# Optimization experiments

Measured on AMD Instinct MI355X. Metric: run time of the kernel, lower is better.

Reference implementation:

```python
import jax, jax.numpy as jnp
import numpy as np

B, N, E, D, H, L = 1024, 64, 1024, 128, 4, 2
C = D // H          # per-head out_channels
K = 5               # options per attribute
LN_EPS = 1e-5


def setup_inputs() -> dict:
    key = jax.random.key(0)
    ks = jax.random.split(key, 22)
    s = 0.05
    inp = {
        'x': jax.random.randint(ks[0], (B, N), 0, K),
        'edge_index': jax.random.randint(ks[1], (2, E), 0, N),
        'edge_attr': jax.random.uniform(ks[2], (E, 1), jnp.float32),
        # tokenizer params
        'attr_emb': jax.random.normal(ks[3], (N, D), jnp.float32) * s,
        'opt_emb': jax.random.normal(ks[4], (N, K, D), jnp.float32) * s,
        'prior': jnp.ones((N, 1), jnp.float32),
        # GATv2 params, stacked over layers
        'Wl': jax.random.normal(ks[5], (L, D, D), jnp.float32) * s,
        'bl': jnp.zeros((L, D), jnp.float32),
        'Wr': jax.random.normal(ks[6], (L, D, D), jnp.float32) * s,
        'br': jnp.zeros((L, D), jnp.float32),
        'We': jax.random.normal(ks[7], (L, 1, D), jnp.float32) * s,
        'att': jax.random.normal(ks[8], (L, H, C), jnp.float32) * s,
        'conv_bias': jnp.zeros((L, D), jnp.float32),
        'ln_g': jnp.ones((L, D), jnp.float32),
        'ln_b': jnp.zeros((L, D), jnp.float32),
        # reliability head
        'W1': jax.random.normal(ks[9], (2 * D, D), jnp.float32) * s,
        'b1': jnp.zeros((D,), jnp.float32),
        'W2': jax.random.normal(ks[10], (D, 1), jnp.float32) * s,
        'b2': jnp.zeros((1,), jnp.float32),
    }
    return inp


def _forward(x, edge_index, edge_attr, attr_emb, opt_emb, prior,
             Wl, bl, Wr, br, We, att, conv_bias, ln_g, ln_b, W1, b1, W2, b2):
    Bb, n = x.shape
    # Tokenizer: token_i = p_i * (E_attr[i] + E_val[i](x_i))
    val = opt_emb[jnp.arange(n)[None, :], x]                 # [B,n,D]
    T0 = (attr_emb[None] + val) * prior[None]                # [B,n,D]

    src, dst = edge_index[0], edge_index[1]
    h = T0
    for l in range(Wl.shape[0]):
        xl = (h @ Wl[l] + bl[l]).reshape(Bb, n, H, C)        # source transform
        xr = (h @ Wr[l] + br[l]).reshape(Bb, n, H, C)        # target transform
        e = (edge_attr @ We[l]).reshape(1, E, H, C)          # edge embedding
        msg = xl[:, src]                                     # [B,E,H,C]
        z = jax.nn.leaky_relu(msg + xr[:, dst] + e, 0.2)
        alpha = jnp.einsum('behc,hc->beh', z, att[l])        # [B,E,H]
        # segment softmax over incoming edges per target node
        mx = jnp.full((Bb, n, H), -jnp.inf, alpha.dtype).at[:, dst].max(alpha)
        ex = jnp.exp(alpha - mx[:, dst])
        den = jnp.zeros((Bb, n, H), alpha.dtype).at[:, dst].add(ex)
        a = ex / den[:, dst]                                 # normalized attention
        out = jnp.zeros((Bb, n, H, C), h.dtype).at[:, dst].add(msg * a[..., None])
        g = out.reshape(Bb, n, D) + conv_bias[l]
        mu = g.mean(-1, keepdims=True)
        var = g.var(-1, keepdims=True)
        g = (g - mu) / jnp.sqrt(var + LN_EPS) * ln_g[l] + ln_b[l]
        g = jax.nn.elu(g)
        h = h + g                                            # residual

    hat_T = jnp.concatenate([T0, h], axis=-1)                # [B,n,2D]
    rel = jax.nn.sigmoid(jax.nn.relu(hat_T @ W1 + b1) @ W2 + b2)[..., 0]  # [B,n]
    rw = rel[..., None]
    f_scale = (h * rw).sum(1) / (rw.sum(1) + 1e-8)           # [B,D]
    return f_scale, rel, hat_T


def reference(x, edge_index, edge_attr, attr_emb, opt_emb, prior,
              Wl, bl, Wr, br, We, att, conv_bias, ln_g, ln_b, W1, b1, W2, b2):
    return _forward(x, edge_index, edge_attr, attr_emb, opt_emb, prior,
                    Wl, bl, Wr, br, We, att, conv_bias, ln_g, ln_b, W1, b1, W2, b2)
```

## Files before the change

kernel.cpp:

```cpp
#include <hip/hip_runtime.h>
#include <hip/hip_bf16.h>

#define Bv 1024
#define Nv 64
#define Ev 1024
#define Dv 128
#define Hv 4
#define Lv 2
#define Kv 5
#define PAD 130

typedef __hip_bfloat16 bf16;
typedef __attribute__((ext_vector_type(8))) short bf16x8_t;
typedef __attribute__((ext_vector_type(4))) float f32x4_t;
typedef __attribute__((ext_vector_type(2))) float f32x2_t;

__device__ __forceinline__ float b2f(bf16 v) { return __bfloat162float(v); }
__device__ __forceinline__ bf16  f2b(float v) { return __float2bfloat16(v); }

__device__ bf16 g_pWl[(size_t)Lv * 2 * Dv * Dv];
__device__ bf16 g_pWr[(size_t)Lv * 2 * Dv * Dv];
__device__ bf16 g_pW1[(size_t)2 * 2 * Dv * Dv];
__device__ float g_K[Lv * Hv];

__device__ __forceinline__ void unpack2(unsigned int u, float& lo, float& hi) {
    union { unsigned int u; float f; } a, b;
    a.u = u << 16;
    b.u = u & 0xffff0000u;
    lo = a.f; hi = b.f;
}

__device__ __forceinline__ f32x2_t unpack2v(unsigned int u) {
    union { unsigned int u; float f; } a, b;
    a.u = u << 16;
    b.u = u & 0xffff0000u;
    return (f32x2_t){a.f, b.f};
}

__device__ __forceinline__ unsigned int pack2v(f32x2_t v) {
    union { bf16 b; unsigned short u; } lo, hi;
    lo.b = f2b(v.x); hi.b = f2b(v.y);
    return (unsigned int)lo.u | ((unsigned int)hi.u << 16);
}

__device__ __forceinline__ bf16x8_t load_a_frag(const bf16* buf, int elem_idx) {
    const unsigned int* p = (const unsigned int*)buf;
    union { bf16x8_t v; unsigned int u[4]; } r;
    int d = elem_idx >> 1;
    r.u[0] = p[d]; r.u[1] = p[d + 1]; r.u[2] = p[d + 2]; r.u[3] = p[d + 3];
    return r.v;
}

__device__ void pack_mat(const float* __restrict__ W, bf16* __restrict__ out,
                         int K, int tid, int nth)
{
    const int total = K * 128;
    for (int e = tid; e < total; e += nth) {
        int f    = e >> 9;
        int rem  = e & 511;
        int lane = rem >> 3;
        int i    = rem & 7;
        int kk   = f >> 3;
        int nt   = f & 7;
        int col  = nt * 16 + (lane & 15);
        int k    = kk * 32 + (lane >> 4) * 8 + i;
        float w  = W[k * 128 + col];
        bf16 hi  = f2b(w);
        out[e]         = hi;
        out[total + e] = f2b(w - b2f(hi));
    }
}

__global__ void prep(const int* __restrict__ edge_index,
                     int* __restrict__ off, int* __restrict__ eid,
                     const float* __restrict__ Wl, const float* __restrict__ Wr,
                     const float* __restrict__ W1, const float* __restrict__ We,
                     const float* __restrict__ att)
{
    const int bid = blockIdx.x;
    if (bid == 0) {
        __shared__ int cnt[Nv];
        int tid = threadIdx.x;
        if (tid < Nv) cnt[tid] = 0;
        __syncthreads();
        for (int e = tid; e < Ev; e += blockDim.x)
            atomicAdd(&cnt[edge_index[Ev + e]], 1);
        __syncthreads();
        if (tid == 0) {
            int s = 0;
            for (int t = 0; t < Nv; ++t) { int c = cnt[t]; off[t] = s; cnt[t] = s; s += c; }
            off[Nv] = s;
        }
        __syncthreads();
        for (int e = tid; e < Ev; e += blockDim.x) {
            int d = edge_index[Ev + e];
            int pos = atomicAdd(&cnt[d], 1);
            eid[pos] = e;
        }
        return;
    }
    const int nth = 64 * 256;
    const int tid = (bid - 1) * 256 + threadIdx.x;
    for (int l = 0; l < Lv; ++l) {
        pack_mat(Wl + (size_t)l * Dv * Dv, g_pWl + (size_t)l * 2 * Dv * Dv, Dv, tid, nth);
        pack_mat(Wr + (size_t)l * Dv * Dv, g_pWr + (size_t)l * 2 * Dv * Dv, Dv, tid, nth);
    }
    pack_mat(W1, g_pW1, 2 * Dv, tid, nth);
    if (bid == 1 && threadIdx.x < Lv * Hv) {
        int l = threadIdx.x / Hv, h = threadIdx.x % Hv;
        float k = 0.f;
        for (int c = 0; c < 32; ++c)
            k += att[l * Dv + h * 32 + c] * We[l * Dv + h * 32 + c];
        g_K[threadIdx.x] = 0.2f * k;
    }
}

__global__ __launch_bounds__(512, 2)
void gat_fused(const int* __restrict__ x, const int* __restrict__ edge_index,
               const float* __restrict__ edge_attr, const float* __restrict__ attr_emb,
               const float* __restrict__ opt_emb, const float* __restrict__ prior,
               const float* __restrict__ bl, const float* __restrict__ br,
               const float* __restrict__ conv_bias, const float* __restrict__ ln_g,
               const float* __restrict__ ln_b,
               const float* __restrict__ b1, const float* __restrict__ W2,
               const float* __restrict__ b2,
               const float* __restrict__ We, const float* __restrict__ att,
               const int* __restrict__ csr_off, const int* __restrict__ csr_eid,
               float* __restrict__ out_fscale, float* __restrict__ out_rel,
               float* __restrict__ out_hatT)
{
    const int b = blockIdx.x;
    const int tid = threadIdx.x;

    __shared__ __align__(16) bf16 hs [Nv * PAD];
    __shared__ __align__(16) bf16 xls[Nv * PAD];
    __shared__ __align__(16) bf16 xrs[Nv * PAD];
    __shared__ bf16 alphas[Ev * Hv];
    __shared__ __align__(16) float red [Nv * 8];
    __shared__ __align__(16) float red2[Nv * 8];
    __shared__ __align__(16) float wecol[Dv];
    __shared__ __align__(16) float attv [Dv];
    __shared__ float relbuf[Nv];

    for (int idx = tid; idx < Nv * Dv; idx += 512) {
        int n = idx >> 7, d = idx & 127;
        float t0 = (attr_emb[n * Dv + d] + opt_emb[(n * Kv + x[b * Nv + n]) * Dv + d])
                   * prior[n];
        hs[n * PAD + d] = f2b(t0);
    }

    for (int l = 0; l < Lv; ++l) {
        if (tid < Dv) {
            wecol[tid] = We[l * Dv + tid];
            attv[tid]  = att[l * Dv + tid];
        }
        __syncthreads();

        {
            const int w = tid >> 6, lane = tid & 63;
            const int row16 = lane & 15, kg = lane >> 4;
            const bf16* pB = (w < 4) ? (g_pWl + (size_t)l * 2 * Dv * Dv)
                                     : (g_pWr + (size_t)l * 2 * Dv * Dv);
            const int wc = (w & 3) * 32;
            f32x4_t acc[4][2];
            #pragma unroll
            for (int mt = 0; mt < 4; ++mt)
                #pragma unroll
                for (int nt = 0; nt < 2; ++nt)
                    acc[mt][nt] = (f32x4_t){0.f, 0.f, 0.f, 0.f};

            #pragma unroll
            for (int kk = 0; kk < 4; ++kk) {
                const int kb = kk * 32 + kg * 8;
                bf16x8_t a[4];
                #pragma unroll
                for (int mt = 0; mt < 4; ++mt)
                    a[mt] = load_a_frag(hs, (mt * 16 + row16) * PAD + kb);
                #pragma unroll
                for (int nt = 0; nt < 2; ++nt) {
                    const int f = kk * 8 + (w & 3) * 2 + nt;
                    bf16x8_t bh  = *(const bf16x8_t*)&pB[(size_t)(f * 64 + lane) * 8];
                    bf16x8_t blo = *(const bf16x8_t*)&pB[Dv * Dv + (size_t)(f * 64 + lane) * 8];
                    #pragma unroll
                    for (int mt = 0; mt < 4; ++mt) {
                        acc[mt][nt] = __builtin_amdgcn_mfma_f32_16x16x32_bf16(
                                          a[mt], bh, acc[mt][nt], 0, 0, 0);
                        acc[mt][nt] = __builtin_amdgcn_mfma_f32_16x16x32_bf16(
                                          a[mt], blo, acc[mt][nt], 0, 0, 0);
                    }
                }
            }
            bf16* dst = (w < 4) ? xls : xrs;
            const float* bias = (w < 4) ? (bl + l * Dv) : (br + l * Dv);
            #pragma unroll
            for (int mt = 0; mt < 4; ++mt)
                #pragma unroll
                for (int nt = 0; nt < 2; ++nt) {
                    const int col = wc + nt * 16 + row16;
                    #pragma unroll
                    for (int r = 0; r < 4; ++r) {
                        const int row = mt * 16 + kg * 4 + r;
                        dst[row * PAD + col] = f2b(acc[mt][nt][r] + bias[col]);
                    }
                }
        }
        __syncthreads();

        {
            const int t = tid & 63, h = (tid >> 6) & 3, half = tid >> 8;
            const int ch0 = h * 32 + half * 16;
            f32x2_t dl2 = {0.f, 0.f}, dr2 = {0.f, 0.f};
            #pragma unroll
            for (int c = 0; c < 16; c += 2) {
                f32x2_t a2 = *(const f32x2_t*)&attv[ch0 + c];
                dl2 += a2 * unpack2v(*(const unsigned int*)&xls[t * PAD + ch0 + c]);
                dr2 += a2 * unpack2v(*(const unsigned int*)&xrs[t * PAD + ch0 + c]);
            }
            red [t * 8 + h * 2 + half] = dl2.x + dl2.y;
            red2[t * 8 + h * 2 + half] = dr2.x + dr2.y;
        }
        __syncthreads();

        {
            const int h = (tid >> 6) & 3, half = tid >> 8, lane = tid & 63;
            const float k02 = g_K[l * Hv + h];
            const f32x2_t zero2 = {0.f, 0.f};
            for (int it = 0; it < 8; ++it) {
                int e = (half * 8 + it) * 64 + lane;
                int s = edge_index[e], t = edge_index[Ev + e];
                float ea = edge_attr[e];
                f32x2_t ea2 = {ea, ea};
                f32x2_t acc2 = {0.f, 0.f};
                int bs = s * PAD + h * 32, bt = t * PAD + h * 32;
                #pragma unroll
                for (int c = 0; c < 32; c += 2) {
                    f32x2_t xl2 = unpack2v(*(const unsigned int*)&xls[bs + c]);
                    f32x2_t xr2 = unpack2v(*(const unsigned int*)&xrs[bt + c]);
                    f32x2_t we2 = *(const f32x2_t*)&wecol[h * 32 + c];
                    f32x2_t at2 = *(const f32x2_t*)&attv [h * 32 + c];
                    f32x2_t v   = xl2 + xr2 + ea2 * we2;
                    acc2 += at2 * __builtin_elementwise_max(v, zero2);
                }
                float dL = red [s * 8 + h * 2] + red [s * 8 + h * 2 + 1];
                float dR = red2[t * 8 + h * 2] + red2[t * 8 + h * 2 + 1];
                float alpha = 0.2f * (dL + dR) + k02 * ea + 0.8f * (acc2.x + acc2.y);
                alphas[e * Hv + h] = f2b(alpha);
            }
        }
        __syncthreads();

        {
            const int t = tid & 63, h = (tid >> 6) & 3, half = tid >> 8;
            const int ch0 = h * 32 + half * 16;
            int beg = csr_off[t], end = csr_off[t + 1];
            float mx = -3e38f;
            for (int idx = beg; idx < end; ++idx)
                mx = fmaxf(mx, b2f(alphas[csr_eid[idx] * Hv + h]));
            f32x2_t acc2[8];
            #pragma unroll
            for (int j = 0; j < 8; ++j) acc2[j] = (f32x2_t){0.f, 0.f};
            float den = 0.f;
            for (int idx = beg; idx < end; ++idx) {
                int e = csr_eid[idx];
                int s = edge_index[e];
                float ex = expf(b2f(alphas[e * Hv + h]) - mx);
                den += ex;
                f32x2_t ex2 = {ex, ex};
                int bs = s * PAD + ch0;
                #pragma unroll
                for (int j = 0; j < 8; ++j)
                    acc2[j] += ex2 * unpack2v(*(const unsigned int*)&xls[bs + 2 * j]);
            }
            float inv_den = (end > beg) ? 1.f / den : 0.f;
            f32x2_t id2 = {inv_den, inv_den};
            f32x2_t sum2 = {0.f, 0.f}, sq2 = {0.f, 0.f};
            #pragma unroll
            for (int j = 0; j < 8; ++j) {
                f32x2_t cb = *(const f32x2_t*)&conv_bias[l * Dv + ch0 + 2 * j];
                f32x2_t g  = acc2[j] * id2 + cb;
                acc2[j] = g;
                sum2 += g; sq2 += g * g;
            }
            red [t * 8 + h * 2 + half] = sum2.x + sum2.y;
            red2[t * 8 + h * 2 + half] = sq2.x + sq2.y;
            __syncthreads();
            float mu = 0.f, ms = 0.f;
            #pragma unroll
            for (int j = 0; j < 8; ++j) { mu += red[t * 8 + j]; ms += red2[t * 8 + j]; }
            mu *= (1.f / 128.f); ms *= (1.f / 128.f);
            float rstd = rsqrtf(ms - mu * mu + 1e-5f);
            f32x2_t mu2 = {mu, mu}, rs2 = {rstd, rstd};
            #pragma unroll
            for (int j = 0; j < 8; ++j) {
                f32x2_t lg = *(const f32x2_t*)&ln_g[l * Dv + ch0 + 2 * j];
                f32x2_t lb = *(const f32x2_t*)&ln_b[l * Dv + ch0 + 2 * j];
                f32x2_t g  = (acc2[j] - mu2) * rs2 * lg + lb;
                g.x = g.x > 0.f ? g.x : (expf(g.x) - 1.f);
                g.y = g.y > 0.f ? g.y : (expf(g.y) - 1.f);
                unsigned int* hp = (unsigned int*)&hs[t * PAD + ch0 + 2 * j];
                f32x2_t hv = unpack2v(*hp) + g;
                *hp = pack2v(hv);
            }
        }
        __syncthreads();
    }

    if (tid < Dv) wecol[tid] = W2[tid];
    for (int idx = tid; idx < Nv * Dv; idx += 512) {
        int n = idx >> 7, d = idx & 127;
        float t0 = (attr_emb[n * Dv + d] + opt_emb[(n * Kv + x[b * Nv + n]) * Dv + d])
                   * prior[n];
        xrs[n * PAD + d] = f2b(t0);
        size_t rb = ((size_t)(b * Nv + n)) * (2 * Dv);
        out_hatT[rb + d]      = t0;
        out_hatT[rb + Dv + d] = b2f(hs[n * PAD + d]);
    }
    __syncthreads();

    {
        const int w = tid >> 6, lane = tid & 63;
        const int row16 = lane & 15, kg = lane >> 4;
        f32x4_t acc[4];
        #pragma unroll
        for (int mt = 0; mt < 4; ++mt)
            acc[mt] = (f32x4_t){0.f, 0.f, 0.f, 0.f};

        #pragma unroll
        for (int kk = 0; kk < 8; ++kk) {
            const bf16* asrc = (kk < 4) ? xrs : hs;
            const int kb = (kk & 3) * 32 + kg * 8;
            bf16x8_t a[4];
            #pragma unroll
            for (int mt = 0; mt < 4; ++mt)
                a[mt] = load_a_frag(asrc, (mt * 16 + row16) * PAD + kb);
            const int f = kk * 8 + w;
            bf16x8_t bh  = *(const bf16x8_t*)&g_pW1[(size_t)(f * 64 + lane) * 8];
            bf16x8_t blo = *(const bf16x8_t*)&g_pW1[(size_t)2 * Dv * Dv + (size_t)(f * 64 + lane) * 8];
            #pragma unroll
            for (int mt = 0; mt < 4; ++mt) {
                acc[mt] = __builtin_amdgcn_mfma_f32_16x16x32_bf16(a[mt], bh,  acc[mt], 0, 0, 0);
                acc[mt] = __builtin_amdgcn_mfma_f32_16x16x32_bf16(a[mt], blo, acc[mt], 0, 0, 0);
            }
        }
        #pragma unroll
        for (int mt = 0; mt < 4; ++mt) {
            const int col = w * 16 + row16;
            #pragma unroll
            for (int r = 0; r < 4; ++r) {
                const int row = mt * 16 + kg * 4 + r;
                float v = acc[mt][r] + b1[col];
                xls[row * PAD + col] = f2b(v > 0.f ? v : 0.f);
            }
        }
    }
    __syncthreads();

    {
        const int t = tid & 63, h = (tid >> 6) & 3, half = tid >> 8;
        const int ch0 = h * 32 + half * 16;
        f32x2_t s2 = {0.f, 0.f};
        #pragma unroll
        for (int c = 0; c < 16; c += 2) {
            f32x2_t h2 = unpack2v(*(const unsigned int*)&xls[t * PAD + ch0 + c]);
            s2 += h2 * *(const f32x2_t*)&wecol[ch0 + c];
        }
        red[t * 8 + h * 2 + half] = s2.x + s2.y;
        __syncthreads();
        if (h == 0 && half == 0) {
            float z = b2[0];
            #pragma unroll
            for (int j = 0; j < 8; ++j) z += red[t * 8 + j];
            float r = 1.f / (1.f + expf(-z));
            relbuf[t] = r;
            out_rel[b * Nv + t] = r;
        }
    }
    __syncthreads();

    if (tid < Dv) {
        float num = 0.f, den = 0.f;
        for (int n = 0; n < Nv; ++n) {
            float r = relbuf[n];
            num += b2f(hs[n * PAD + tid]) * r;
            den += r;
        }
        out_fscale[b * Dv + tid] = num / (den + 1e-8f);
    }
}

extern "C" void kernel_launch(void* const* d_in, const int* in_sizes, int n_in,
                              void* d_out, int out_size, void* d_ws, size_t ws_size,
                              hipStream_t stream)
{
    const int*   x          = (const int*)  d_in[0];
    const int*   edge_index = (const int*)  d_in[1];
    const float* edge_attr  = (const float*)d_in[2];
    const float* attr_emb   = (const float*)d_in[3];
    const float* opt_emb    = (const float*)d_in[4];
    const float* prior      = (const float*)d_in[5];
    const float* Wl         = (const float*)d_in[6];
    const float* bl         = (const float*)d_in[7];
    const float* Wr         = (const float*)d_in[8];
    const float* br         = (const float*)d_in[9];
    const float* We         = (const float*)d_in[10];
    const float* att        = (const float*)d_in[11];
    const float* conv_bias  = (const float*)d_in[12];
    const float* ln_g       = (const float*)d_in[13];
    const float* ln_b       = (const float*)d_in[14];
    const float* W1         = (const float*)d_in[15];
    const float* b1         = (const float*)d_in[16];
    const float* W2         = (const float*)d_in[17];
    const float* b2         = (const float*)d_in[18];

    int* csr_off = (int*)d_ws;
    int* csr_eid = (int*)d_ws + 128;

    float* out        = (float*)d_out;
    float* out_fscale = out;
    float* out_rel    = out + (size_t)Bv * Dv;
    float* out_hatT   = out + (size_t)Bv * Dv + (size_t)Bv * Nv;

    prep<<<65, 256, 0, stream>>>(edge_index, csr_off, csr_eid, Wl, Wr, W1, We, att);
    gat_fused<<<Bv, 512, 0, stream>>>(x, edge_index, edge_attr, attr_emb, opt_emb,
                                      prior, bl, br, conv_bias,
                                      ln_g, ln_b, b1, W2, b2, We, att,
                                      csr_off, csr_eid,
                                      out_fscale, out_rel, out_hatT);
}
```

Measured before the change: 302.7 us.

## Pre-sort edges by destination with packed src/dst and cache in shared memory

The prep kernel now writes edges in destination-sorted order as packed 16-bit src|dst codes plus reordered edge attributes. The main kernel copies these into shared memory once per block. The alpha and aggregation phases then index by sorted position, which removes the csr_eid indirection and the global edge_index and edge_attr loads inside the per-layer loops. The prep grid is also doubled to spread weight packing across more blocks, at the cost of extra shared memory per block that may pressure occupancy.

```diff
diff --git a/kernel.cpp b/kernel.cpp
--- a/kernel.cpp
+++ b/kernel.cpp
@@ -22,13 +22,9 @@
 __device__ bf16 g_pWr[(size_t)Lv * 2 * Dv * Dv];
 __device__ bf16 g_pW1[(size_t)2 * 2 * Dv * Dv];
 __device__ float g_K[Lv * Hv];
-
-__device__ __forceinline__ void unpack2(unsigned int u, float& lo, float& hi) {
-    union { unsigned int u; float f; } a, b;
-    a.u = u << 16;
-    b.u = u & 0xffff0000u;
-    lo = a.f; hi = b.f;
-}
+__device__ unsigned short g_spk[Ev];
+__device__ float          g_sea[Ev];
+__device__ int            g_off[Nv + 1];
 
 __device__ __forceinline__ f32x2_t unpack2v(unsigned int u) {
     union { unsigned int u; float f; } a, b;
@@ -71,8 +67,7 @@
     }
 }
 
-__global__ void prep(const int* __restrict__ edge_index,
-                     int* __restrict__ off, int* __restrict__ eid,
+__global__ void prep(const int* __restrict__ edge_index, const float* __restrict__ edge_attr,
                      const float* __restrict__ Wl, const float* __restrict__ Wr,
                      const float* __restrict__ W1, const float* __restrict__ We,
                      const float* __restrict__ att)
@@ -88,18 +83,20 @@
         __syncthreads();
         if (tid == 0) {
             int s = 0;
-            for (int t = 0; t < Nv; ++t) { int c = cnt[t]; off[t] = s; cnt[t] = s; s += c; }
-            off[Nv] = s;
+            for (int t = 0; t < Nv; ++t) { int c = cnt[t]; g_off[t] = s; cnt[t] = s; s += c; }
+            g_off[Nv] = s;
         }
         __syncthreads();
         for (int e = tid; e < Ev; e += blockDim.x) {
+            int s = edge_index[e];
             int d = edge_index[Ev + e];
             int pos = atomicAdd(&cnt[d], 1);
-            eid[pos] = e;
+            g_spk[pos] = (unsigned short)(s | (d << 6));
+            g_sea[pos] = edge_attr[e];
         }
         return;
     }
-    const int nth = 64 * 256;
+    const int nth = (gridDim.x - 1) * 256;
     const int tid = (bid - 1) * 256 + threadIdx.x;
     for (int l = 0; l < Lv; ++l) {
         pack_mat(Wl + (size_t)l * Dv * Dv, g_pWl + (size_t)l * 2 * Dv * Dv, Dv, tid, nth);
@@ -116,8 +113,8 @@
 }
 
 __global__ __launch_bounds__(512, 2)
-void gat_fused(const int* __restrict__ x, const int* __restrict__ edge_index,
-               const float* __restrict__ edge_attr, const float* __restrict__ attr_emb,
+void gat_fused(const int* __restrict__ x,
+               const float* __restrict__ attr_emb,
                const float* __restrict__ opt_emb, const float* __restrict__ prior,
                const float* __restrict__ bl, const float* __restrict__ br,
                const float* __restrict__ conv_bias, const float* __restrict__ ln_g,
@@ -125,7 +122,6 @@
                const float* __restrict__ b1, const float* __restrict__ W2,
                const float* __restrict__ b2,
                const float* __restrict__ We, const float* __restrict__ att,
-               const int* __restrict__ csr_off, const int* __restrict__ csr_eid,
                float* __restrict__ out_fscale, float* __restrict__ out_rel,
                float* __restrict__ out_hatT)
 {
@@ -141,7 +137,15 @@
     __shared__ __align__(16) float wecol[Dv];
     __shared__ __align__(16) float attv [Dv];
     __shared__ float relbuf[Nv];
-
+    __shared__ __align__(16) unsigned short spk[Ev];
+    __shared__ __align__(16) float sea[Ev];
+    __shared__ int off[Nv + 1];
+
+    for (int i = tid; i < Ev; i += 512) {
+        spk[i] = g_spk[i];
+        sea[i] = g_sea[i];
+    }
+    if (tid < Nv + 1) off[tid] = g_off[tid];
     for (int idx = tid; idx < Nv * Dv; idx += 512) {
         int n = idx >> 7, d = idx & 127;
         float t0 = (attr_emb[n * Dv + d] + opt_emb[(n * Kv + x[b * Nv + n]) * Dv + d])
@@ -226,9 +230,10 @@
             const float k02 = g_K[l * Hv + h];
             const f32x2_t zero2 = {0.f, 0.f};
             for (int it = 0; it < 8; ++it) {
-                int e = (half * 8 + it) * 64 + lane;
-                int s = edge_index[e], t = edge_index[Ev + e];
-                float ea = edge_attr[e];
+                int pos = (half * 8 + it) * 64 + lane;
+                int pk = spk[pos];
+                int s = pk & 63, t = (pk >> 6) & 63;
+                float ea = sea[pos];
                 f32x2_t ea2 = {ea, ea};
                 f32x2_t acc2 = {0.f, 0.f};
                 int bs = s * PAD + h * 32, bt = t * PAD + h * 32;
@@ -244,7 +249,7 @@
                 float dL = red [s * 8 + h * 2] + red [s * 8 + h * 2 + 1];
                 float dR = red2[t * 8 + h * 2] + red2[t * 8 + h * 2 + 1];
                 float alpha = 0.2f * (dL + dR) + k02 * ea + 0.8f * (acc2.x + acc2.y);
-                alphas[e * Hv + h] = f2b(alpha);
+                alphas[pos * Hv + h] = f2b(alpha);
             }
         }
         __syncthreads();
@@ -252,18 +257,17 @@
         {
             const int t = tid & 63, h = (tid >> 6) & 3, half = tid >> 8;
             const int ch0 = h * 32 + half * 16;
-            int beg = csr_off[t], end = csr_off[t + 1];
+            int beg = off[t], end = off[t + 1];
             float mx = -3e38f;
             for (int idx = beg; idx < end; ++idx)
-                mx = fmaxf(mx, b2f(alphas[csr_eid[idx] * Hv + h]));
+                mx = fmaxf(mx, b2f(alphas[idx * Hv + h]));
             f32x2_t acc2[8];
             #pragma unroll
             for (int j = 0; j < 8; ++j) acc2[j] = (f32x2_t){0.f, 0.f};
             float den = 0.f;
             for (int idx = beg; idx < end; ++idx) {
-                int e = csr_eid[idx];
-                int s = edge_index[e];
-                float ex = expf(b2f(alphas[e * Hv + h]) - mx);
+                int s = spk[idx] & 63;
+                float ex = expf(b2f(alphas[idx * Hv + h]) - mx);
                 den += ex;
                 f32x2_t ex2 = {ex, ex};
                 int bs = s * PAD + ch0;
@@ -412,18 +416,14 @@
     const float* W2         = (const float*)d_in[17];
     const float* b2         = (const float*)d_in[18];
 
-    int* csr_off = (int*)d_ws;
-    int* csr_eid = (int*)d_ws + 128;
-
     float* out        = (float*)d_out;
     float* out_fscale = out;
     float* out_rel    = out + (size_t)Bv * Dv;
     float* out_hatT   = out + (size_t)Bv * Dv + (size_t)Bv * Nv;
 
-    prep<<<65, 256, 0, stream>>>(edge_index, csr_off, csr_eid, Wl, Wr, W1, We, att);
-    gat_fused<<<Bv, 512, 0, stream>>>(x, edge_index, edge_attr, attr_emb, opt_emb,
+    prep<<<129, 256, 0, stream>>>(edge_index, edge_attr, Wl, Wr, W1, We, att);
+    gat_fused<<<Bv, 512, 0, stream>>>(x, attr_emb, opt_emb,
                                       prior, bl, br, conv_bias,
                                       ln_g, ln_b, b1, W2, b2, We, att,
-                                      csr_off, csr_eid,
                                       out_fscale, out_rel, out_hatT);
 }
```

After: 281.2 us. 7.1% less time.
